# Kernel optimization log

Hardware: AMD Instinct MI355X
Metric: run time of the kernel (lower is better)

The kernel has to match this reference:

```python
import jax, jax.numpy as jnp
import numpy as np

D_MODEL = 2048
N_EXPERTS = 8
TOP_K = 2
FFN_HIDDEN = int(D_MODEL * 1.5)  # 3072, matches int(d_model*1.5)


def setup_inputs() -> dict:
    key = jax.random.key(0)
    k_x, k_r, k_g, k_u, k_d = jax.random.split(key, 5)
    B, L = 4, 4096
    s_in = 1.0 / np.sqrt(D_MODEL)
    s_hid = 1.0 / np.sqrt(FFN_HIDDEN)
    return {
        "x": jax.random.normal(k_x, (B, L, D_MODEL), dtype=jnp.float32),
        # nn.Linear weights are stored (out_features, in_features)
        "router_w": jax.random.uniform(k_r, (N_EXPERTS, D_MODEL), jnp.float32, -s_in, s_in),
        "gate_w": jax.random.uniform(k_g, (N_EXPERTS, FFN_HIDDEN, D_MODEL), jnp.float32, -s_in, s_in),
        "up_w": jax.random.uniform(k_u, (N_EXPERTS, FFN_HIDDEN, D_MODEL), jnp.float32, -s_in, s_in),
        "down_w": jax.random.uniform(k_d, (N_EXPERTS, D_MODEL, FFN_HIDDEN), jnp.float32, -s_hid, s_hid),
    }


def reference(x, router_w, gate_w, up_w, down_w):
    B, L, D = x.shape
    x_flat = x.reshape(-1, D)                                   # [N, D]

    router_logits = x_flat @ router_w.T                          # [N, E]
    router_probs = jax.nn.softmax(router_logits, axis=-1)
    top_k_probs, top_k_idx = jax.lax.top_k(router_probs, TOP_K)  # [N, K]
    top_k_probs = top_k_probs / jnp.sum(top_k_probs, axis=-1, keepdims=True)

    # combine[n, e] = sum_k top_k_probs[n,k] * (top_k_idx[n,k] == e)
    onehot = jax.nn.one_hot(top_k_idx, N_EXPERTS, dtype=x.dtype)  # [N, K, E]
    combine = jnp.einsum("nk,nke->ne", top_k_probs, onehot)       # [N, E]

    # Masked gather/scatter in the original == weight-0 tokens here; same math.
    output = jnp.zeros_like(x_flat)
    for e in range(N_EXPERTS):
        gate = jax.nn.silu(x_flat @ gate_w[e].T)                  # [N, H]
        up = x_flat @ up_w[e].T                                   # [N, H]
        expert_out = (gate * up) @ down_w[e].T                    # [N, D]
        output = output + combine[:, e:e + 1] * expert_out

    # dropout is identity in eval/reference mode
    return output.reshape(B, L, D)
```

## Files before the change

### kernel.cpp

```cpp
#include <hip/hip_runtime.h>
#include <hip/hip_bf16.h>
#include <cstdint>

#define N_TOK 16384
#define DMODEL 2048
#define FFH    3072
#define NGU    (2 * FFH)
#define NEXP   8
#define ATOT   32768

typedef __bf16 bf16;
typedef __attribute__((ext_vector_type(8))) __bf16 bf16x8;
typedef __attribute__((ext_vector_type(4))) __bf16 bf16x4;
typedef __attribute__((ext_vector_type(4))) float  f32x4;

__device__ __forceinline__ void gl_lds16(const bf16* g, void* l) {
  __builtin_amdgcn_global_load_lds(
      (const __attribute__((address_space(1))) void*)g,
      (__attribute__((address_space(3))) void*)l, 16, 0, 0);
}

__global__ void cvt_f32_bf16(const float* __restrict__ src, bf16* __restrict__ dst, long n4) {
  long i = (long)blockIdx.x * blockDim.x + threadIdx.x;
  if (i >= n4) return;
  const float4 v = ((const float4*)src)[i];
  bf16x4 o;
  o.x = (bf16)v.x; o.y = (bf16)v.y; o.z = (bf16)v.z; o.w = (bf16)v.w;
  ((bf16x4*)dst)[i] = o;
}

__global__ void cvt_guw(const float* __restrict__ gw, const float* __restrict__ uw,
                        bf16* __restrict__ guw) {
  const long i = (long)blockIdx.x * 256 + threadIdx.x;
  const int c8 = (int)(i & 255);
  const long rg = i >> 8;
  const int e = (int)(rg / NGU);
  const int ri = (int)(rg - (long)e * NGU);
  const int hb = ri >> 6, sub = ri & 63;
  const float* src = (sub < 32 ? gw : uw) + ((size_t)e * FFH + hb * 32 + (sub & 31)) * DMODEL + c8 * 8;
  const float4 v0 = ((const float4*)src)[0];
  const float4 v1 = ((const float4*)src)[1];
  bf16x8 o;
  o[0] = (bf16)v0.x; o[1] = (bf16)v0.y; o[2] = (bf16)v0.z; o[3] = (bf16)v0.w;
  o[4] = (bf16)v1.x; o[5] = (bf16)v1.y; o[6] = (bf16)v1.z; o[7] = (bf16)v1.w;
  *(bf16x8*)(guw + rg * DMODEL + c8 * 8) = o;
}

__global__ void router_k(const float* __restrict__ x, const float* __restrict__ rw,
                         bf16* __restrict__ xb,
                         int* __restrict__ tk_e, float* __restrict__ tk_w,
                         int* __restrict__ cnt) {
  const int wv = threadIdx.x >> 6, lane = threadIdx.x & 63;
  const int t = blockIdx.x * 4 + wv;
  const float4* xr = (const float4*)(x + (size_t)t * DMODEL);
  bf16x4* xbr = (bf16x4*)(xb + (size_t)t * DMODEL);
  float acc[NEXP];
#pragma unroll
  for (int e = 0; e < NEXP; ++e) acc[e] = 0.f;
#pragma unroll
  for (int it = 0; it < DMODEL / 4 / 64; ++it) {
    const int idx = lane + it * 64;
    const float4 v = xr[idx];
    bf16x4 o;
    o.x = (bf16)v.x; o.y = (bf16)v.y; o.z = (bf16)v.z; o.w = (bf16)v.w;
    xbr[idx] = o;
#pragma unroll
    for (int e = 0; e < NEXP; ++e) {
      const float4 w = ((const float4*)(rw + e * DMODEL))[idx];
      acc[e] = fmaf(v.x, w.x, fmaf(v.y, w.y, fmaf(v.z, w.z, fmaf(v.w, w.w, acc[e]))));
    }
  }
#pragma unroll
  for (int e = 0; e < NEXP; ++e) {
#pragma unroll
    for (int o = 32; o; o >>= 1) acc[e] += __shfl_xor(acc[e], o, 64);
  }
  if (lane == 0) {
    int e0 = 0; float v0 = acc[0];
#pragma unroll
    for (int e = 1; e < NEXP; ++e) if (acc[e] > v0) { v0 = acc[e]; e0 = e; }
    int e1 = -1; float v1 = -1e30f;
#pragma unroll
    for (int e = 0; e < NEXP; ++e) if (e != e0 && acc[e] > v1) { v1 = acc[e]; e1 = e; }
    const float w0 = 1.f / (1.f + __expf(v1 - v0));
    tk_e[t * 2] = e0; tk_e[t * 2 + 1] = e1;
    tk_w[t * 2] = w0; tk_w[t * 2 + 1] = 1.f - w0;
    atomicAdd(&cnt[e0], 1); atomicAdd(&cnt[e1], 1);
  }
}

__global__ void offs_k(const int* __restrict__ cnt, int* __restrict__ offs) {
  if (threadIdx.x == 0) {
    int o = 0;
    for (int e = 0; e < NEXP; ++e) { offs[e] = o; o += cnt[e]; }
  }
}

__global__ void scatter_k(const int* __restrict__ tk_e, const float* __restrict__ tk_w,
                          const int* __restrict__ offs, int* __restrict__ cnt2,
                          int* __restrict__ tok_list, float* __restrict__ w_list,
                          int* __restrict__ aidx) {
  const int t = blockIdx.x * 256 + threadIdx.x;
  if (t >= N_TOK) return;
#pragma unroll
  for (int k = 0; k < 2; ++k) {
    const int e = tk_e[t * 2 + k];
    const int p = atomicAdd(&cnt2[e], 1);
    const int a = offs[e] + p;
    tok_list[a] = t;
    w_list[a] = tk_w[t * 2 + k];
    aidx[t * 2 + k] = a;
  }
}


__global__ __launch_bounds__(512, 2) void gemm_gu(
    const bf16* __restrict__ A, const bf16* __restrict__ B,
    bf16* __restrict__ hbuf, const int* __restrict__ tok_list,
    const int* __restrict__ cnt, const int* __restrict__ offs) {
  constexpr int NT = DMODEL / 32;
  const int e = blockIdx.z;
  const int cn = cnt[e];
  const int mbase = blockIdx.y * 256;
  if (mbase >= cn) return;
  const int offE = offs[e];
  const int nbase = blockIdx.x * 256;

  __shared__ char lds[98304];
  char* const ldsA = lds;
  char* const ldsB = lds + 49152;

  const int tid = threadIdx.x;
  const int wv = tid >> 6, lane = tid & 63;
  const int wr = wv >> 2, wc = wv & 3;

  const int sr = tid >> 2;
  const int swz8 = ((tid & 3) ^ ((tid >> 3) & 3)) * 8;
  const int t0 = tok_list[offE + min(mbase + sr, cn - 1)];
  const int t1 = tok_list[offE + min(mbase + 128 + sr, cn - 1)];
  const bf16* pA[2] = { A + (size_t)t0 * DMODEL + swz8, A + (size_t)t1 * DMODEL + swz8 };
  const bf16* pB[2] = { B + ((size_t)e * NGU + nbase + sr) * DMODEL + swz8,
                        B + ((size_t)e * NGU + nbase + 128 + sr) * DMODEL + swz8 };

  const int stageDst = wv * 1024;
  const int rswz = ((lane >> 4) ^ ((lane >> 1) & 3)) * 16;
  const int arow = (wr * 128 + (lane & 15)) * 64 + rswz;
  const int brow = (wc * 64 + (lane & 15)) * 64 + rswz;

  const f32x4 zero = {0.f, 0.f, 0.f, 0.f};
  f32x4 acc[8][4];
#pragma unroll
  for (int i = 0; i < 8; ++i)
#pragma unroll
    for (int j = 0; j < 4; ++j) acc[i][j] = zero;

  auto stage_half = [&](int buf, int qh, int kt) {
    const int k8 = kt * 32;
    if (qh < 2) gl_lds16(pA[qh] + k8, ldsA + buf * 16384 + qh * 8192 + stageDst);
    else        gl_lds16(pB[qh - 2] + k8, ldsB + buf * 16384 + (qh - 2) * 8192 + stageDst);
  };

#pragma unroll
  for (int qh = 0; qh < 4; ++qh) stage_half(0, qh, 0);
#pragma unroll
  for (int qh = 0; qh < 4; ++qh) stage_half(1, qh, 1);
  asm volatile("s_waitcnt vmcnt(4)" ::: "memory");
  __builtin_amdgcn_s_barrier();
  asm volatile("" ::: "memory");

  int cb = 0;
  for (int kt = 0; kt < NT; ++kt) {
    const int sb = (cb + 2 >= 3) ? cb - 1 : cb + 2;
    const char* cA = ldsA + cb * 16384;
    const char* cB = ldsB + cb * 16384;

    bf16x8 a[8], b[4];
#pragma unroll
    for (int i = 0; i < 4; ++i) {
      a[i] = *(const bf16x8*)(cA + i * 1024 + arow);
      b[i] = *(const bf16x8*)(cB + i * 1024 + brow);
    }
#pragma unroll
    for (int i = 4; i < 8; ++i) a[i] = *(const bf16x8*)(cA + i * 1024 + arow);

    if (kt + 2 < NT) { stage_half(sb, 0, kt + 2); stage_half(sb, 1, kt + 2); }

    __builtin_amdgcn_s_setprio(1);
#pragma unroll
    for (int nf = 0; nf < 4; ++nf)
#pragma unroll
      for (int mi = 0; mi < 4; ++mi)
        acc[mi][nf] = __builtin_amdgcn_mfma_f32_16x16x32_bf16(a[mi], b[nf], acc[mi][nf], 0, 0, 0);
    __builtin_amdgcn_s_setprio(0);

    if (kt + 2 < NT) { stage_half(sb, 2, kt + 2); stage_half(sb, 3, kt + 2); }

    __builtin_amdgcn_s_setprio(1);
#pragma unroll
    for (int nf = 0; nf < 4; ++nf)
#pragma unroll
      for (int mi = 4; mi < 8; ++mi)
        acc[mi][nf] = __builtin_amdgcn_mfma_f32_16x16x32_bf16(a[mi], b[nf], acc[mi][nf], 0, 0, 0);
    __builtin_amdgcn_s_setprio(0);

    if (kt + 2 < NT) { asm volatile("s_waitcnt vmcnt(4)" ::: "memory"); }
    else             { asm volatile("s_waitcnt vmcnt(0)" ::: "memory"); }
    asm volatile("" ::: "memory");
    __builtin_amdgcn_s_barrier();
    asm volatile("" ::: "memory");

    cb = (cb + 1 == 3) ? 0 : cb + 1;
  }

  const int col = lane & 15;
  const int rb = mbase + wr * 128 + (lane >> 4) * 4;
  const int hb32 = ((nbase + wc * 64) >> 6) * 32;
#pragma unroll
  for (int mi = 0; mi < 8; ++mi)
#pragma unroll
    for (int j = 0; j < 4; ++j) {
      const int row = rb + mi * 16 + j;
      if (row < cn) {
        bf16* hr = hbuf + (size_t)(offE + row) * FFH + hb32 + col;
#pragma unroll
        for (int k = 0; k < 2; ++k) {
          const float g = acc[mi][k][j], u = acc[mi][k + 2][j];
          hr[k * 16] = (bf16)(g / (1.f + __expf(-g)) * u);
        }
      }
    }
}

__global__ __launch_bounds__(512, 2) void gemm_dn(
    const bf16* __restrict__ A, const bf16* __restrict__ B,
    bf16* __restrict__ ybuf, const float* __restrict__ w_list,
    const int* __restrict__ cnt, const int* __restrict__ offs) {
  constexpr int NT = FFH / 32;
  const int e = blockIdx.z;
  const int cn = cnt[e];
  const int mbase = blockIdx.y * 256;
  if (mbase >= cn) return;
  const int offE = offs[e];
  const int nbase = blockIdx.x * 256;

  __shared__ char lds[98304];
  char* const ldsA = lds;
  char* const ldsB = lds + 49152;

  const int tid = threadIdx.x;
  const int wv = tid >> 6, lane = tid & 63;
  const int wr = wv >> 2, wc = wv & 3;

  const int sr = tid >> 2;
  const int swz8 = ((tid & 3) ^ ((tid >> 3) & 3)) * 8;
  const int a0 = offE + min(mbase + sr, cn - 1);
  const int a1 = offE + min(mbase + 128 + sr, cn - 1);
  const bf16* pA[2] = { A + (size_t)a0 * FFH + swz8, A + (size_t)a1 * FFH + swz8 };
  const bf16* pB[2] = { B + ((size_t)e * DMODEL + nbase + sr) * FFH + swz8,
                        B + ((size_t)e * DMODEL + nbase + 128 + sr) * FFH + swz8 };

  const int stageDst = wv * 1024;
  const int rswz = ((lane >> 4) ^ ((lane >> 1) & 3)) * 16;
  const int arow = (wr * 128 + (lane & 15)) * 64 + rswz;
  const int brow = (wc * 64 + (lane & 15)) * 64 + rswz;

  const f32x4 zero = {0.f, 0.f, 0.f, 0.f};
  f32x4 acc[8][4];
#pragma unroll
  for (int i = 0; i < 8; ++i)
#pragma unroll
    for (int j = 0; j < 4; ++j) acc[i][j] = zero;

  auto stage_half = [&](int buf, int qh, int kt) {
    const int k8 = kt * 32;
    if (qh < 2) gl_lds16(pA[qh] + k8, ldsA + buf * 16384 + qh * 8192 + stageDst);
    else        gl_lds16(pB[qh - 2] + k8, ldsB + buf * 16384 + (qh - 2) * 8192 + stageDst);
  };

#pragma unroll
  for (int qh = 0; qh < 4; ++qh) stage_half(0, qh, 0);
#pragma unroll
  for (int qh = 0; qh < 4; ++qh) stage_half(1, qh, 1);
  asm volatile("s_waitcnt vmcnt(4)" ::: "memory");
  __builtin_amdgcn_s_barrier();
  asm volatile("" ::: "memory");

  int cb = 0;
  for (int kt = 0; kt < NT; ++kt) {
    const int sb = (cb + 2 >= 3) ? cb - 1 : cb + 2;
    const char* cA = ldsA + cb * 16384;
    const char* cB = ldsB + cb * 16384;

    bf16x8 a[8], b[4];
#pragma unroll
    for (int i = 0; i < 4; ++i) {
      a[i] = *(const bf16x8*)(cA + i * 1024 + arow);
      b[i] = *(const bf16x8*)(cB + i * 1024 + brow);
    }
#pragma unroll
    for (int i = 4; i < 8; ++i) a[i] = *(const bf16x8*)(cA + i * 1024 + arow);

    if (kt + 2 < NT) { stage_half(sb, 0, kt + 2); stage_half(sb, 1, kt + 2); }

    __builtin_amdgcn_s_setprio(1);
#pragma unroll
    for (int nf = 0; nf < 4; ++nf)
#pragma unroll
      for (int mi = 0; mi < 4; ++mi)
        acc[mi][nf] = __builtin_amdgcn_mfma_f32_16x16x32_bf16(a[mi], b[nf], acc[mi][nf], 0, 0, 0);
    __builtin_amdgcn_s_setprio(0);

    if (kt + 2 < NT) { stage_half(sb, 2, kt + 2); stage_half(sb, 3, kt + 2); }

    __builtin_amdgcn_s_setprio(1);
#pragma unroll
    for (int nf = 0; nf < 4; ++nf)
#pragma unroll
      for (int mi = 4; mi < 8; ++mi)
        acc[mi][nf] = __builtin_amdgcn_mfma_f32_16x16x32_bf16(a[mi], b[nf], acc[mi][nf], 0, 0, 0);
    __builtin_amdgcn_s_setprio(0);

    if (kt + 2 < NT) { asm volatile("s_waitcnt vmcnt(4)" ::: "memory"); }
    else             { asm volatile("s_waitcnt vmcnt(0)" ::: "memory"); }
    asm volatile("" ::: "memory");
    __builtin_amdgcn_s_barrier();
    asm volatile("" ::: "memory");

    cb = (cb + 1 == 3) ? 0 : cb + 1;
  }

  const int col = lane & 15;
  const int rb = mbase + wr * 128 + (lane >> 4) * 4;
#pragma unroll
  for (int mi = 0; mi < 8; ++mi)
#pragma unroll
    for (int j = 0; j < 4; ++j) {
      const int row = rb + mi * 16 + j;
      if (row < cn) {
        const float wg = w_list[offE + row];
        bf16* yr = ybuf + (size_t)(offE + row) * DMODEL + nbase + wc * 64 + col;
#pragma unroll
        for (int nf = 0; nf < 4; ++nf) yr[nf * 16] = (bf16)(wg * acc[mi][nf][j]);
      }
    }
}

__global__ void combine_k(const bf16* __restrict__ ybuf, const int* __restrict__ aidx,
                          float* __restrict__ out) {
  const int i = blockIdx.x * 256 + threadIdx.x;
  const int t = i >> 8, c = i & 255;
  const int a0 = aidx[t * 2], a1 = aidx[t * 2 + 1];
  const bf16x8 v0 = ((const bf16x8*)(ybuf + (size_t)a0 * DMODEL))[c];
  const bf16x8 v1 = ((const bf16x8*)(ybuf + (size_t)a1 * DMODEL))[c];
  float4 o0, o1;
  o0.x = (float)v0[0] + (float)v1[0];
  o0.y = (float)v0[1] + (float)v1[1];
  o0.z = (float)v0[2] + (float)v1[2];
  o0.w = (float)v0[3] + (float)v1[3];
  o1.x = (float)v0[4] + (float)v1[4];
  o1.y = (float)v0[5] + (float)v1[5];
  o1.z = (float)v0[6] + (float)v1[6];
  o1.w = (float)v0[7] + (float)v1[7];
  float4* op = (float4*)(out + (size_t)t * DMODEL + c * 8);
  op[0] = o0; op[1] = o1;
}

extern "C" void kernel_launch(void* const* d_in, const int* in_sizes, int n_in,
                              void* d_out, int out_size, void* d_ws, size_t ws_size,
                              hipStream_t stream) {
  const float* x  = (const float*)d_in[0];
  const float* rw = (const float*)d_in[1];
  const float* gw = (const float*)d_in[2];
  const float* uw = (const float*)d_in[3];
  const float* dw = (const float*)d_in[4];
  float* out = (float*)d_out;

  char* ws = (char*)d_ws;
  size_t o = 0;
  auto alloc = [&](size_t bytes) {
    void* p = ws + o;
    o = (o + bytes + 255) & ~(size_t)255;
    return p;
  };

  const size_t guw_bytes  = (size_t)NEXP * NGU * DMODEL * 2;
  const size_t ybuf_bytes = (size_t)(ATOT + 256) * DMODEL * 2;
  bf16*  xb       = (bf16*)alloc((size_t)N_TOK * DMODEL * 2);
  void*  uni      = alloc(guw_bytes > ybuf_bytes ? guw_bytes : ybuf_bytes);
  bf16*  guw      = (bf16*)uni;
  bf16*  ybuf     = (bf16*)uni;
  bf16*  dwb      = (bf16*)alloc((size_t)NEXP * DMODEL * FFH * 2);
  bf16*  hbuf     = (bf16*)alloc((size_t)(ATOT + 256) * FFH * 2);
  int*   tok_list = (int*)alloc((ATOT + 256) * 4);
  float* w_list   = (float*)alloc((ATOT + 256) * 4);
  int*   tk_e     = (int*)alloc((size_t)N_TOK * 2 * 4);
  float* tk_w     = (float*)alloc((size_t)N_TOK * 2 * 4);
  int*   aidx     = (int*)alloc((size_t)N_TOK * 2 * 4);
  int*   cnt      = (int*)alloc(64);
  int*   offs     = (int*)alloc(64);
  int*   cnt2     = (int*)alloc(64);

  hipMemsetAsync(cnt, 0, 64, stream);
  hipMemsetAsync(cnt2, 0, 64, stream);

  router_k<<<N_TOK / 4, 256, 0, stream>>>(x, rw, xb, tk_e, tk_w, cnt);
  offs_k<<<1, 64, 0, stream>>>(cnt, offs);
  scatter_k<<<N_TOK / 256, 256, 0, stream>>>(tk_e, tk_w, offs, cnt2, tok_list, w_list, aidx);

  cvt_guw<<<(unsigned)((long)NEXP * NGU * DMODEL / 8 / 256), 256, 0, stream>>>(gw, uw, guw);
  {
    long n4 = (long)NEXP * DMODEL * FFH / 4;
    cvt_f32_bf16<<<(unsigned)(n4 / 256), 256, 0, stream>>>(dw, dwb, n4);
  }

  gemm_gu<<<dim3(NGU / 256, 64, NEXP), 512, 0, stream>>>(
      xb, guw, hbuf, tok_list, cnt, offs);
  gemm_dn<<<dim3(DMODEL / 256, 64, NEXP), 512, 0, stream>>>(
      hbuf, dwb, ybuf, w_list, cnt, offs);

  combine_k<<<N_TOK, 256, 0, stream>>>(ybuf, aidx, out);
}
```

Measured before the change: 1.928 ms.

## Switch expert GEMMs to 128x256 tiles with 256-thread blocks

Both expert GEMMs now use 128-row by 256-column block tiles with 4 waves, each wave computing a 64x128 sub-tile instead of 128x64. B is staged in four 64-row chunks and the grid doubles along the token dimension. The aim is finer granularity over ragged per-expert token counts and a different per-wave fragment shape. The cost is less B-tile reuse per block, more staging loads per thread and fewer waves per CU.

```diff
diff --git a/kernel.cpp b/kernel.cpp
--- a/kernel.cpp
+++ b/kernel.cpp
@@ -114,76 +114,78 @@
 }
 
 
-__global__ __launch_bounds__(512, 2) void gemm_gu(
+__global__ __launch_bounds__(256, 2) void gemm_gu(
     const bf16* __restrict__ A, const bf16* __restrict__ B,
     bf16* __restrict__ hbuf, const int* __restrict__ tok_list,
     const int* __restrict__ cnt, const int* __restrict__ offs) {
   constexpr int NT = DMODEL / 32;
   const int e = blockIdx.z;
   const int cn = cnt[e];
-  const int mbase = blockIdx.y * 256;
+  const int mbase = blockIdx.y * 128;
   if (mbase >= cn) return;
   const int offE = offs[e];
   const int nbase = blockIdx.x * 256;
 
-  __shared__ char lds[98304];
+  __shared__ char lds[73728];
   char* const ldsA = lds;
-  char* const ldsB = lds + 49152;
+  char* const ldsB = lds + 24576;
 
   const int tid = threadIdx.x;
   const int wv = tid >> 6, lane = tid & 63;
-  const int wr = wv >> 2, wc = wv & 3;
+  const int wr = wv >> 1, wc = wv & 1;
 
   const int sr = tid >> 2;
   const int swz8 = ((tid & 3) ^ ((tid >> 3) & 3)) * 8;
   const int t0 = tok_list[offE + min(mbase + sr, cn - 1)];
-  const int t1 = tok_list[offE + min(mbase + 128 + sr, cn - 1)];
+  const int t1 = tok_list[offE + min(mbase + 64 + sr, cn - 1)];
   const bf16* pA[2] = { A + (size_t)t0 * DMODEL + swz8, A + (size_t)t1 * DMODEL + swz8 };
-  const bf16* pB[2] = { B + ((size_t)e * NGU + nbase + sr) * DMODEL + swz8,
-                        B + ((size_t)e * NGU + nbase + 128 + sr) * DMODEL + swz8 };
+  const bf16* pB[4];
+#pragma unroll
+  for (int h = 0; h < 4; ++h)
+    pB[h] = B + ((size_t)e * NGU + nbase + h * 64 + sr) * DMODEL + swz8;
 
   const int stageDst = wv * 1024;
   const int rswz = ((lane >> 4) ^ ((lane >> 1) & 3)) * 16;
-  const int arow = (wr * 128 + (lane & 15)) * 64 + rswz;
-  const int brow = (wc * 64 + (lane & 15)) * 64 + rswz;
+  const int arow = (wr * 64 + (lane & 15)) * 64 + rswz;
+  const int brow = (wc * 128 + (lane & 15)) * 64 + rswz;
 
   const f32x4 zero = {0.f, 0.f, 0.f, 0.f};
-  f32x4 acc[8][4];
-#pragma unroll
-  for (int i = 0; i < 8; ++i)
-#pragma unroll
-    for (int j = 0; j < 4; ++j) acc[i][j] = zero;
-
-  auto stage_half = [&](int buf, int qh, int kt) {
+  f32x4 acc[4][8];
+#pragma unroll
+  for (int i = 0; i < 4; ++i)
+#pragma unroll
+    for (int j = 0; j < 8; ++j) acc[i][j] = zero;
+
+  auto stage = [&](int buf, int qh, int kt) {
     const int k8 = kt * 32;
-    if (qh < 2) gl_lds16(pA[qh] + k8, ldsA + buf * 16384 + qh * 8192 + stageDst);
-    else        gl_lds16(pB[qh - 2] + k8, ldsB + buf * 16384 + (qh - 2) * 8192 + stageDst);
+    if (qh < 2) gl_lds16(pA[qh] + k8, ldsA + buf * 8192 + qh * 4096 + stageDst);
+    else        gl_lds16(pB[qh - 2] + k8, ldsB + buf * 16384 + (qh - 2) * 4096 + stageDst);
   };
 
 #pragma unroll
-  for (int qh = 0; qh < 4; ++qh) stage_half(0, qh, 0);
-#pragma unroll
-  for (int qh = 0; qh < 4; ++qh) stage_half(1, qh, 1);
-  asm volatile("s_waitcnt vmcnt(4)" ::: "memory");
+  for (int qh = 0; qh < 6; ++qh) stage(0, qh, 0);
+#pragma unroll
+  for (int qh = 0; qh < 6; ++qh) stage(1, qh, 1);
+  asm volatile("s_waitcnt vmcnt(6)" ::: "memory");
   __builtin_amdgcn_s_barrier();
   asm volatile("" ::: "memory");
 
   int cb = 0;
   for (int kt = 0; kt < NT; ++kt) {
     const int sb = (cb + 2 >= 3) ? cb - 1 : cb + 2;
-    const char* cA = ldsA + cb * 16384;
+    const char* cA = ldsA + cb * 8192;
     const char* cB = ldsB + cb * 16384;
 
-    bf16x8 a[8], b[4];
+    bf16x8 a[4], b[8];
 #pragma unroll
     for (int i = 0; i < 4; ++i) {
       a[i] = *(const bf16x8*)(cA + i * 1024 + arow);
       b[i] = *(const bf16x8*)(cB + i * 1024 + brow);
     }
 #pragma unroll
-    for (int i = 4; i < 8; ++i) a[i] = *(const bf16x8*)(cA + i * 1024 + arow);
-
-    if (kt + 2 < NT) { stage_half(sb, 0, kt + 2); stage_half(sb, 1, kt + 2); }
+    for (int i = 4; i < 8; ++i) b[i] = *(const bf16x8*)(cB + i * 1024 + brow);
+
+    if (kt + 2 < NT) { stage(sb, 0, kt + 2); stage(sb, 1, kt + 2); stage(sb, 2, kt + 2); }
 
     __builtin_amdgcn_s_setprio(1);
 #pragma unroll
@@ -193,17 +195,17 @@
         acc[mi][nf] = __builtin_amdgcn_mfma_f32_16x16x32_bf16(a[mi], b[nf], acc[mi][nf], 0, 0, 0);
     __builtin_amdgcn_s_setprio(0);
 
-    if (kt + 2 < NT) { stage_half(sb, 2, kt + 2); stage_half(sb, 3, kt + 2); }
+    if (kt + 2 < NT) { stage(sb, 3, kt + 2); stage(sb, 4, kt + 2); stage(sb, 5, kt + 2); }
 
     __builtin_amdgcn_s_setprio(1);
 #pragma unroll
-    for (int nf = 0; nf < 4; ++nf)
-#pragma unroll
-      for (int mi = 4; mi < 8; ++mi)
+    for (int nf = 4; nf < 8; ++nf)
+#pragma unroll
+      for (int mi = 0; mi < 4; ++mi)
         acc[mi][nf] = __builtin_amdgcn_mfma_f32_16x16x32_bf16(a[mi], b[nf], acc[mi][nf], 0, 0, 0);
     __builtin_amdgcn_s_setprio(0);
 
-    if (kt + 2 < NT) { asm volatile("s_waitcnt vmcnt(4)" ::: "memory"); }
+    if (kt + 2 < NT) { asm volatile("s_waitcnt vmcnt(6)" ::: "memory"); }
     else             { asm volatile("s_waitcnt vmcnt(0)" ::: "memory"); }
     asm volatile("" ::: "memory");
     __builtin_amdgcn_s_barrier();
@@ -213,94 +215,99 @@
   }
 
   const int col = lane & 15;
-  const int rb = mbase + wr * 128 + (lane >> 4) * 4;
-  const int hb32 = ((nbase + wc * 64) >> 6) * 32;
-#pragma unroll
-  for (int mi = 0; mi < 8; ++mi)
+  const int rb = mbase + wr * 64 + (lane >> 4) * 4;
+#pragma unroll
+  for (int mi = 0; mi < 4; ++mi)
 #pragma unroll
     for (int j = 0; j < 4; ++j) {
       const int row = rb + mi * 16 + j;
       if (row < cn) {
-        bf16* hr = hbuf + (size_t)(offE + row) * FFH + hb32 + col;
-#pragma unroll
-        for (int k = 0; k < 2; ++k) {
-          const float g = acc[mi][k][j], u = acc[mi][k + 2][j];
-          hr[k * 16] = (bf16)(g / (1.f + __expf(-g)) * u);
+        bf16* hrow = hbuf + (size_t)(offE + row) * FFH;
+#pragma unroll
+        for (int b2 = 0; b2 < 2; ++b2) {
+          const int hb32 = ((nbase + wc * 128 + b2 * 64) >> 6) * 32;
+#pragma unroll
+          for (int k = 0; k < 2; ++k) {
+            const float g = acc[mi][b2 * 4 + k][j], u = acc[mi][b2 * 4 + 2 + k][j];
+            hrow[hb32 + col + k * 16] = (bf16)(g / (1.f + __expf(-g)) * u);
+          }
         }
       }
     }
 }
 
-__global__ __launch_bounds__(512, 2) void gemm_dn(
+__global__ __launch_bounds__(256, 2) void gemm_dn(
     const bf16* __restrict__ A, const bf16* __restrict__ B,
     bf16* __restrict__ ybuf, const float* __restrict__ w_list,
     const int* __restrict__ cnt, const int* __restrict__ offs) {
   constexpr int NT = FFH / 32;
   const int e = blockIdx.z;
   const int cn = cnt[e];
-  const int mbase = blockIdx.y * 256;
+  const int mbase = blockIdx.y * 128;
   if (mbase >= cn) return;
   const int offE = offs[e];
   const int nbase = blockIdx.x * 256;
 
-  __shared__ char lds[98304];
+  __shared__ char lds[73728];
   char* const ldsA = lds;
-  char* const ldsB = lds + 49152;
+  char* const ldsB = lds + 24576;
 
   const int tid = threadIdx.x;
   const int wv = tid >> 6, lane = tid & 63;
-  const int wr = wv >> 2, wc = wv & 3;
+  const int wr = wv >> 1, wc = wv & 1;
 
   const int sr = tid >> 2;
   const int swz8 = ((tid & 3) ^ ((tid >> 3) & 3)) * 8;
   const int a0 = offE + min(mbase + sr, cn - 1);
-  const int a1 = offE + min(mbase + 128 + sr, cn - 1);
+  const int a1 = offE + min(mbase + 64 + sr, cn - 1);
   const bf16* pA[2] = { A + (size_t)a0 * FFH + swz8, A + (size_t)a1 * FFH + swz8 };
-  const bf16* pB[2] = { B + ((size_t)e * DMODEL + nbase + sr) * FFH + swz8,
-                        B + ((size_t)e * DMODEL + nbase + 128 + sr) * FFH + swz8 };
+  const bf16* pB[4];
+#pragma unroll
+  for (int h = 0; h < 4; ++h)
+    pB[h] = B + ((size_t)e * DMODEL + nbase + h * 64 + sr) * FFH + swz8;
 
   const int stageDst = wv * 1024;
   const int rswz = ((lane >> 4) ^ ((lane >> 1) & 3)) * 16;
-  const int arow = (wr * 128 + (lane & 15)) * 64 + rswz;
-  const int brow = (wc * 64 + (lane & 15)) * 64 + rswz;
+  const int arow = (wr * 64 + (lane & 15)) * 64 + rswz;
+  const int brow = (wc * 128 + (lane & 15)) * 64 + rswz;
 
   const f32x4 zero = {0.f, 0.f, 0.f, 0.f};
-  f32x4 acc[8][4];
-#pragma unroll
-  for (int i = 0; i < 8; ++i)
-#pragma unroll
-    for (int j = 0; j < 4; ++j) acc[i][j] = zero;
-
-  auto stage_half = [&](int buf, int qh, int kt) {
+  f32x4 acc[4][8];
+#pragma unroll
+  for (int i = 0; i < 4; ++i)
+#pragma unroll
+    for (int j = 0; j < 8; ++j) acc[i][j] = zero;
+
+  auto stage = [&](int buf, int qh, int kt) {
     const int k8 = kt * 32;
-    if (qh < 2) gl_lds16(pA[qh] + k8, ldsA + buf * 16384 + qh * 8192 + stageDst);
-    else        gl_lds16(pB[qh - 2] + k8, ldsB + buf * 16384 + (qh - 2) * 8192 + stageDst);
+    if (qh < 2) gl_lds16(pA[qh] + k8, ldsA + buf * 8192 + qh * 4096 + stageDst);
+    else        gl_lds16(pB[qh - 2] + k8, ldsB + buf * 16384 + (qh - 2) * 4096 + stageDst);
   };
 
 #pragma unroll
-  for (int qh = 0; qh < 4; ++qh) stage_half(0, qh, 0);
-#pragma unroll
-  for (int qh = 0; qh < 4; ++qh) stage_half(1, qh, 1);
-  asm volatile("s_waitcnt vmcnt(4)" ::: "memory");
+  for (int qh = 0; qh < 6; ++qh) stage(0, qh, 0);
+#pragma unroll
+  for (int qh = 0; qh < 6; ++qh) stage(1, qh, 1);
+  asm volatile("s_waitcnt vmcnt(6)" ::: "memory");
   __builtin_amdgcn_s_barrier();
   asm volatile("" ::: "memory");
 
   int cb = 0;
   for (int kt = 0; kt < NT; ++kt) {
     const int sb = (cb + 2 >= 3) ? cb - 1 : cb + 2;
-    const char* cA = ldsA + cb * 16384;
+    const char* cA = ldsA + cb * 8192;
     const char* cB = ldsB + cb * 16384;
 
-    bf16x8 a[8], b[4];
+    bf16x8 a[4], b[8];
 #pragma unroll
     for (int i = 0; i < 4; ++i) {
       a[i] = *(const bf16x8*)(cA + i * 1024 + arow);
       b[i] = *(const bf16x8*)(cB + i * 1024 + brow);
     }
 #pragma unroll
-    for (int i = 4; i < 8; ++i) a[i] = *(const bf16x8*)(cA + i * 1024 + arow);
-
-    if (kt + 2 < NT) { stage_half(sb, 0, kt + 2); stage_half(sb, 1, kt + 2); }
+    for (int i = 4; i < 8; ++i) b[i] = *(const bf16x8*)(cB + i * 1024 + brow);
+
+    if (kt + 2 < NT) { stage(sb, 0, kt + 2); stage(sb, 1, kt + 2); stage(sb, 2, kt + 2); }
 
     __builtin_amdgcn_s_setprio(1);
 #pragma unroll
@@ -310,17 +317,17 @@
         acc[mi][nf] = __builtin_amdgcn_mfma_f32_16x16x32_bf16(a[mi], b[nf], acc[mi][nf], 0, 0, 0);
     __builtin_amdgcn_s_setprio(0);
 
-    if (kt + 2 < NT) { stage_half(sb, 2, kt + 2); stage_half(sb, 3, kt + 2); }
+    if (kt + 2 < NT) { stage(sb, 3, kt + 2); stage(sb, 4, kt + 2); stage(sb, 5, kt + 2); }
 
     __builtin_amdgcn_s_setprio(1);
 #pragma unroll
-    for (int nf = 0; nf < 4; ++nf)
-#pragma unroll
-      for (int mi = 4; mi < 8; ++mi)
+    for (int nf = 4; nf < 8; ++nf)
+#pragma unroll
+      for (int mi = 0; mi < 4; ++mi)
         acc[mi][nf] = __builtin_amdgcn_mfma_f32_16x16x32_bf16(a[mi], b[nf], acc[mi][nf], 0, 0, 0);
     __builtin_amdgcn_s_setprio(0);
 
-    if (kt + 2 < NT) { asm volatile("s_waitcnt vmcnt(4)" ::: "memory"); }
+    if (kt + 2 < NT) { asm volatile("s_waitcnt vmcnt(6)" ::: "memory"); }
     else             { asm volatile("s_waitcnt vmcnt(0)" ::: "memory"); }
     asm volatile("" ::: "memory");
     __builtin_amdgcn_s_barrier();
@@ -330,17 +337,17 @@
   }
 
   const int col = lane & 15;
-  const int rb = mbase + wr * 128 + (lane >> 4) * 4;
-#pragma unroll
-  for (int mi = 0; mi < 8; ++mi)
+  const int rb = mbase + wr * 64 + (lane >> 4) * 4;
+#pragma unroll
+  for (int mi = 0; mi < 4; ++mi)
 #pragma unroll
     for (int j = 0; j < 4; ++j) {
       const int row = rb + mi * 16 + j;
       if (row < cn) {
         const float wg = w_list[offE + row];
-        bf16* yr = ybuf + (size_t)(offE + row) * DMODEL + nbase + wc * 64 + col;
-#pragma unroll
-        for (int nf = 0; nf < 4; ++nf) yr[nf * 16] = (bf16)(wg * acc[mi][nf][j]);
+        bf16* yr = ybuf + (size_t)(offE + row) * DMODEL + nbase + wc * 128 + col;
+#pragma unroll
+        for (int nf = 0; nf < 8; ++nf) yr[nf * 16] = (bf16)(wg * acc[mi][nf][j]);
       }
     }
 }
@@ -413,9 +420,9 @@
     cvt_f32_bf16<<<(unsigned)(n4 / 256), 256, 0, stream>>>(dw, dwb, n4);
   }
 
-  gemm_gu<<<dim3(NGU / 256, 64, NEXP), 512, 0, stream>>>(
+  gemm_gu<<<dim3(NGU / 256, 128, NEXP), 256, 0, stream>>>(
       xb, guw, hbuf, tok_list, cnt, offs);
-  gemm_dn<<<dim3(DMODEL / 256, 64, NEXP), 512, 0, stream>>>(
+  gemm_dn<<<dim3(DMODEL / 256, 128, NEXP), 256, 0, stream>>>(
       hbuf, dwb, ybuf, w_list, cnt, offs);
 
   combine_k<<<N_TOK, 256, 0, stream>>>(ybuf, aidx, out);
```

Result: no change. 1.959 ms (+1.6%).

## Use 4-wave blocks with 128x128 warp tiles in gate/up GEMM

Applied to the files above, without the earlier changes.

The gate/up grouped GEMM now runs 256 threads (4 waves in a 2x2 grid) instead of 512, and each wave computes a 128x128 output tile with 8x8 accumulators. The block tile stays 256x256, and staging issues 8 global-to-LDS loads per thread per k-step. The aim is more MFMA work per LDS fragment read and less per-wave overhead. In exchange, each wave holds about 256 accumulator registers, which lowers occupancy to one block per CU and raises register-spill risk.

```diff
diff --git a/kernel.cpp b/kernel.cpp
--- a/kernel.cpp
+++ b/kernel.cpp
@@ -113,8 +113,7 @@
   }
 }
 
-
-__global__ __launch_bounds__(512, 2) void gemm_gu(
+__global__ __launch_bounds__(256, 1) void gemm_gu(
     const bf16* __restrict__ A, const bf16* __restrict__ B,
     bf16* __restrict__ hbuf, const int* __restrict__ tok_list,
     const int* __restrict__ cnt, const int* __restrict__ offs) {
@@ -132,39 +131,41 @@
 
   const int tid = threadIdx.x;
   const int wv = tid >> 6, lane = tid & 63;
-  const int wr = wv >> 2, wc = wv & 3;
+  const int wr = wv >> 1, wc = wv & 1;
 
   const int sr = tid >> 2;
   const int swz8 = ((tid & 3) ^ ((tid >> 3) & 3)) * 8;
-  const int t0 = tok_list[offE + min(mbase + sr, cn - 1)];
-  const int t1 = tok_list[offE + min(mbase + 128 + sr, cn - 1)];
-  const bf16* pA[2] = { A + (size_t)t0 * DMODEL + swz8, A + (size_t)t1 * DMODEL + swz8 };
-  const bf16* pB[2] = { B + ((size_t)e * NGU + nbase + sr) * DMODEL + swz8,
-                        B + ((size_t)e * NGU + nbase + 128 + sr) * DMODEL + swz8 };
-
-  const int stageDst = wv * 1024;
+  const bf16* pA[4]; const bf16* pB[4];
+#pragma unroll
+  for (int q = 0; q < 4; ++q) {
+    const int tq = tok_list[offE + min(mbase + q * 64 + sr, cn - 1)];
+    pA[q] = A + (size_t)tq * DMODEL + swz8;
+    pB[q] = B + ((size_t)e * NGU + nbase + q * 64 + sr) * DMODEL + swz8;
+  }
+
+  const int stageDst = tid * 16;
   const int rswz = ((lane >> 4) ^ ((lane >> 1) & 3)) * 16;
   const int arow = (wr * 128 + (lane & 15)) * 64 + rswz;
-  const int brow = (wc * 64 + (lane & 15)) * 64 + rswz;
+  const int brow = (wc * 128 + (lane & 15)) * 64 + rswz;
 
   const f32x4 zero = {0.f, 0.f, 0.f, 0.f};
-  f32x4 acc[8][4];
+  f32x4 acc[8][8];
 #pragma unroll
   for (int i = 0; i < 8; ++i)
 #pragma unroll
-    for (int j = 0; j < 4; ++j) acc[i][j] = zero;
-
-  auto stage_half = [&](int buf, int qh, int kt) {
+    for (int j = 0; j < 8; ++j) acc[i][j] = zero;
+
+  auto stage = [&](int buf, int qh, int kt) {
     const int k8 = kt * 32;
-    if (qh < 2) gl_lds16(pA[qh] + k8, ldsA + buf * 16384 + qh * 8192 + stageDst);
-    else        gl_lds16(pB[qh - 2] + k8, ldsB + buf * 16384 + (qh - 2) * 8192 + stageDst);
+    if (qh < 4) gl_lds16(pA[qh] + k8, ldsA + buf * 16384 + qh * 4096 + stageDst);
+    else        gl_lds16(pB[qh - 4] + k8, ldsB + buf * 16384 + (qh - 4) * 4096 + stageDst);
   };
 
 #pragma unroll
-  for (int qh = 0; qh < 4; ++qh) stage_half(0, qh, 0);
-#pragma unroll
-  for (int qh = 0; qh < 4; ++qh) stage_half(1, qh, 1);
-  asm volatile("s_waitcnt vmcnt(4)" ::: "memory");
+  for (int qh = 0; qh < 8; ++qh) stage(0, qh, 0);
+#pragma unroll
+  for (int qh = 0; qh < 8; ++qh) stage(1, qh, 1);
+  asm volatile("s_waitcnt vmcnt(8)" ::: "memory");
   __builtin_amdgcn_s_barrier();
   asm volatile("" ::: "memory");
 
@@ -174,36 +175,40 @@
     const char* cA = ldsA + cb * 16384;
     const char* cB = ldsB + cb * 16384;
 
-    bf16x8 a[8], b[4];
-#pragma unroll
-    for (int i = 0; i < 4; ++i) {
+    bf16x8 a[8], b[8];
+#pragma unroll
+    for (int i = 0; i < 8; ++i) {
       a[i] = *(const bf16x8*)(cA + i * 1024 + arow);
       b[i] = *(const bf16x8*)(cB + i * 1024 + brow);
     }
-#pragma unroll
-    for (int i = 4; i < 8; ++i) a[i] = *(const bf16x8*)(cA + i * 1024 + arow);
-
-    if (kt + 2 < NT) { stage_half(sb, 0, kt + 2); stage_half(sb, 1, kt + 2); }
+
+    if (kt + 2 < NT) {
+      stage(sb, 0, kt + 2); stage(sb, 1, kt + 2);
+      stage(sb, 2, kt + 2); stage(sb, 3, kt + 2);
+    }
 
     __builtin_amdgcn_s_setprio(1);
 #pragma unroll
     for (int nf = 0; nf < 4; ++nf)
 #pragma unroll
-      for (int mi = 0; mi < 4; ++mi)
+      for (int mi = 0; mi < 8; ++mi)
         acc[mi][nf] = __builtin_amdgcn_mfma_f32_16x16x32_bf16(a[mi], b[nf], acc[mi][nf], 0, 0, 0);
     __builtin_amdgcn_s_setprio(0);
 
-    if (kt + 2 < NT) { stage_half(sb, 2, kt + 2); stage_half(sb, 3, kt + 2); }
+    if (kt + 2 < NT) {
+      stage(sb, 4, kt + 2); stage(sb, 5, kt + 2);
+      stage(sb, 6, kt + 2); stage(sb, 7, kt + 2);
+    }
 
     __builtin_amdgcn_s_setprio(1);
 #pragma unroll
-    for (int nf = 0; nf < 4; ++nf)
-#pragma unroll
-      for (int mi = 4; mi < 8; ++mi)
+    for (int nf = 4; nf < 8; ++nf)
+#pragma unroll
+      for (int mi = 0; mi < 8; ++mi)
         acc[mi][nf] = __builtin_amdgcn_mfma_f32_16x16x32_bf16(a[mi], b[nf], acc[mi][nf], 0, 0, 0);
     __builtin_amdgcn_s_setprio(0);
 
-    if (kt + 2 < NT) { asm volatile("s_waitcnt vmcnt(4)" ::: "memory"); }
+    if (kt + 2 < NT) { asm volatile("s_waitcnt vmcnt(8)" ::: "memory"); }
     else             { asm volatile("s_waitcnt vmcnt(0)" ::: "memory"); }
     asm volatile("" ::: "memory");
     __builtin_amdgcn_s_barrier();
@@ -214,18 +219,21 @@
 
   const int col = lane & 15;
   const int rb = mbase + wr * 128 + (lane >> 4) * 4;
-  const int hb32 = ((nbase + wc * 64) >> 6) * 32;
 #pragma unroll
   for (int mi = 0; mi < 8; ++mi)
 #pragma unroll
     for (int j = 0; j < 4; ++j) {
       const int row = rb + mi * 16 + j;
       if (row < cn) {
-        bf16* hr = hbuf + (size_t)(offE + row) * FFH + hb32 + col;
-#pragma unroll
-        for (int k = 0; k < 2; ++k) {
-          const float g = acc[mi][k][j], u = acc[mi][k + 2][j];
-          hr[k * 16] = (bf16)(g / (1.f + __expf(-g)) * u);
+        bf16* hrow = hbuf + (size_t)(offE + row) * FFH;
+#pragma unroll
+        for (int b2 = 0; b2 < 2; ++b2) {
+          const int hb32 = ((nbase + wc * 128 + b2 * 64) >> 6) * 32;
+#pragma unroll
+          for (int k = 0; k < 2; ++k) {
+            const float g = acc[mi][b2 * 4 + k][j], u = acc[mi][b2 * 4 + 2 + k][j];
+            hrow[hb32 + col + k * 16] = (bf16)(g / (1.f + __expf(-g)) * u);
+          }
         }
       }
     }
@@ -413,7 +421,7 @@
     cvt_f32_bf16<<<(unsigned)(n4 / 256), 256, 0, stream>>>(dw, dwb, n4);
   }
 
-  gemm_gu<<<dim3(NGU / 256, 64, NEXP), 512, 0, stream>>>(
+  gemm_gu<<<dim3(NGU / 256, 64, NEXP), 256, 0, stream>>>(
       xb, guw, hbuf, tok_list, cnt, offs);
   gemm_dn<<<dim3(DMODEL / 256, 64, NEXP), 512, 0, stream>>>(
       hbuf, dwb, ybuf, w_list, cnt, offs);
```

New measurement: 3.613 ms. +87.4%, slower.
